# Optimization experiments

Measured on AMD Instinct MI355X. Metric: run time of the kernel, lower is better.

The kernel has to match this reference:

```python
import jax, jax.numpy as jnp
import numpy as np

HID = 32  # hidden channels (hard-coded in module)
K = 2     # kernel size


def conv1d(x, w, b, dilation=1):
    # x: [B, C_in, T], w: [C_out, C_in, K], b: [C_out]
    y = jax.lax.conv_general_dilated(
        x, w, window_strides=(1,), padding='VALID',
        rhs_dilation=(dilation,), dimension_numbers=('NCH', 'OIH', 'NCH'))
    return y + b[None, :, None]


def setup_inputs() -> dict:
    key = jax.random.key(0)
    ks = jax.random.split(key, 24)
    B, T, C_IN, C_OUT = 32, 4096, 64, 448
    s = 0.05
    inp = {
        'x': jax.random.normal(ks[0], (B, T, C_IN), dtype=jnp.float32),
        'w_causal': jax.random.normal(ks[1], (HID, C_IN, K), dtype=jnp.float32) * s,
        'b_causal': jax.random.normal(ks[2], (HID,), dtype=jnp.float32) * s,
        'wd0': jax.random.normal(ks[3], (HID, HID, K), dtype=jnp.float32) * s,
        'bd0': jax.random.normal(ks[4], (HID,), dtype=jnp.float32) * s,
        'ws0': jax.random.normal(ks[5], (HID, HID, 1), dtype=jnp.float32) * s,
        'bs0': jax.random.normal(ks[6], (HID,), dtype=jnp.float32) * s,
        'wo0': jax.random.normal(ks[7], (HID, HID, 1), dtype=jnp.float32) * s,
        'bo0': jax.random.normal(ks[8], (HID,), dtype=jnp.float32) * s,
        'wd1': jax.random.normal(ks[9], (HID, HID, K), dtype=jnp.float32) * s,
        'bd1': jax.random.normal(ks[10], (HID,), dtype=jnp.float32) * s,
        'ws1': jax.random.normal(ks[11], (HID, HID, 1), dtype=jnp.float32) * s,
        'bs1': jax.random.normal(ks[12], (HID,), dtype=jnp.float32) * s,
        'wo1': jax.random.normal(ks[13], (HID, HID, 1), dtype=jnp.float32) * s,
        'bo1': jax.random.normal(ks[14], (HID,), dtype=jnp.float32) * s,
        'w_sk1': jax.random.normal(ks[15], (HID, HID, 1), dtype=jnp.float32) * s,
        'b_sk1': jax.random.normal(ks[16], (HID,), dtype=jnp.float32) * s,
        'w_sk2': jax.random.normal(ks[17], (C_OUT, HID, 1), dtype=jnp.float32) * s,
        'b_sk2': jax.random.normal(ks[18], (C_OUT,), dtype=jnp.float32) * s,
    }
    return inp


def reference(x, w_causal, b_causal,
              wd0, bd0, ws0, bs0, wo0, bo0,
              wd1, bd1, ws1, bs1, wo1, bo1,
              w_sk1, b_sk1, w_sk2, b_sk2):
    # x: [B, T, C_in] -> [B, C_in, T]
    xt = jnp.transpose(x, (0, 2, 1))
    # T (=4096) >= rf_size (=4) so the top-level rf padding branch is a no-op.
    xt = jnp.pad(xt, ((0, 0), (0, 0), (1, 0)))  # causal left-pad of 1
    z = conv1d(xt, w_causal, b_causal)          # [B, HID, T]

    skip = jnp.zeros_like(z)
    blocks = [(wd0, bd0, ws0, bs0, wo0, bo0, 1),
              (wd1, bd1, ws1, bs1, wo1, bo1, 2)]
    for wd, bd, ws, bs, wo, bo, dil in blocks:
        zp = jnp.pad(z, ((0, 0), (0, 0), (dil, 0)))  # causal pad of `dilation`
        g = conv1d(zp, wd, bd, dilation=dil)          # length preserved: T
        g = jnp.tanh(g) * jax.nn.sigmoid(g)           # gated activation
        skip = skip + conv1d(g, ws, bs)               # skip accumulation
        z = conv1d(g, wo, bo) + z                     # residual (x[...,-T:] == z)

    out = jax.nn.relu(skip)
    out = jax.nn.relu(conv1d(out, w_sk1, b_sk1))
    out = conv1d(out, w_sk2, b_sk2)                   # [B, C_out, T]
    return jnp.transpose(out, (0, 2, 1))              # [B, T, C_out]
```

## Files before the change

kernel.cpp:

```cpp
#include <hip/hip_runtime.h>

#define T_LEN 4096
#define NB    32
#define CIN   64
#define CH    32
#define COUT  448
#define COLS  64
#define HALO  3
#define OUTC  (COLS - HALO)
#define BLK_A 256
#define TR_B  16

#define H_ELEMS  (NB * T_LEN * CH)
#define WT_C   0
#define WT_D0  4096
#define WT_D1  6144
#define WT_S0  8192
#define WT_O0  9216
#define WT_S1  10240
#define WT_K1  11264
#define WT_N   12288

__device__ __forceinline__ float gated(float d) {
  float dc = fminf(fmaxf(d, -30.0f), 30.0f);
  float e2 = __expf(-2.0f * dc);
  float th = (1.0f - e2) / (1.0f + e2);
  float sg = 1.0f / (1.0f + __expf(-dc));
  return th * sg;
}

__global__ void dicnn_prep(const float* __restrict__ wc,
    const float* __restrict__ wd0, const float* __restrict__ wd1,
    const float* __restrict__ ws0, const float* __restrict__ wo0,
    const float* __restrict__ ws1, const float* __restrict__ wk1,
    float* __restrict__ wt)
{
  int i = blockIdx.x * 256 + threadIdx.x;
  if (i >= WT_N) return;
  float v;
  if (i < WT_D0) {
    int c = i & 31, k = (i >> 5) & 1, ci = i >> 6;
    v = wc[c * 128 + ci * 2 + k];
  } else if (i < WT_D1) {
    int j = i - WT_D0; int c = j & 31, k = (j >> 5) & 1, ci = j >> 6;
    v = wd0[c * 64 + ci * 2 + k];
  } else if (i < WT_S0) {
    int j = i - WT_D1; int c = j & 31, k = (j >> 5) & 1, ci = j >> 6;
    v = wd1[c * 64 + ci * 2 + k];
  } else if (i < WT_O0) {
    int j = i - WT_S0; int c = j & 31, ci = j >> 5;
    v = ws0[c * 32 + ci];
  } else if (i < WT_S1) {
    int j = i - WT_O0; int c = j & 31, ci = j >> 5;
    v = wo0[c * 32 + ci];
  } else if (i < WT_K1) {
    int j = i - WT_S1; int c = j & 31, ci = j >> 5;
    v = ws1[c * 32 + ci];
  } else {
    int j = i - WT_K1; int c = j & 31, ci = j >> 5;
    v = wk1[c * 32 + ci];
  }
  wt[i] = v;
}

__global__ __launch_bounds__(BLK_A, 4) void dicnn_front(
    const float* __restrict__ x, const float* __restrict__ wt,
    const float* __restrict__ b_causal,
    const float* __restrict__ bd0, const float* __restrict__ bs0,
    const float* __restrict__ bo0, const float* __restrict__ bd1,
    const float* __restrict__ bs1, const float* __restrict__ b_sk1,
    float* __restrict__ h_out)
{
  __shared__ float zbuf[CH][COLS];
  __shared__ float gbuf[CH][COLS];

  const int tid = threadIdx.x;
  const int col = tid & 63;
  const int c0  = __builtin_amdgcn_readfirstlane((tid >> 6) << 3);
  const int b   = blockIdx.y;
  const int t   = blockIdx.x * OUTC - HALO + col;

  const float* wt_c  = wt + WT_C;
  const float* wt_d0 = wt + WT_D0;
  const float* wt_d1 = wt + WT_D1;
  const float* wt_s0 = wt + WT_S0;
  const float* wt_o0 = wt + WT_O0;
  const float* wt_s1 = wt + WT_S1;
  const float* wt_k1 = wt + WT_K1;

  float z0[8];
  #pragma unroll
  for (int c = 0; c < 8; ++c) z0[c] = 0.f;
  if (t >= 0 && t < T_LEN) {
    #pragma unroll
    for (int c = 0; c < 8; ++c) z0[c] = b_causal[c0 + c];
    const float* xr = x + ((size_t)b * T_LEN + t) * CIN;
    for (int ci = 0; ci < CIN; ci += 4) {
      float4 xc = *(const float4*)(xr + ci);
      float4 xp = make_float4(0.f, 0.f, 0.f, 0.f);
      if (t > 0) xp = *(const float4*)(xr - CIN + ci);
      #pragma unroll
      for (int j = 0; j < 4; ++j) {
        const float* wp = wt_c + (ci + j) * 64 + c0;
        const float xpv = (&xp.x)[j];
        const float xcv = (&xc.x)[j];
        #pragma unroll
        for (int c = 0; c < 8; ++c)
          z0[c] += wp[c] * xpv + wp[32 + c] * xcv;
      }
    }
  }
  #pragma unroll
  for (int c = 0; c < 8; ++c) zbuf[c0 + c][col] = z0[c];
  __syncthreads();

  const int cp1 = (col >= 1) ? col - 1 : 0;
  float acc[8];
  #pragma unroll
  for (int c = 0; c < 8; ++c) acc[c] = bd0[c0 + c];
  for (int ci = 0; ci < CH; ++ci) {
    float zp = zbuf[ci][cp1];
    float zc = zbuf[ci][col];
    const float* wp = wt_d0 + ci * 64 + c0;
    #pragma unroll
    for (int c = 0; c < 8; ++c)
      acc[c] += wp[c] * zp + wp[32 + c] * zc;
  }
  #pragma unroll
  for (int c = 0; c < 8; ++c) gbuf[c0 + c][col] = gated(acc[c]);
  __syncthreads();

  float skip[8], z1[8];
  #pragma unroll
  for (int c = 0; c < 8; ++c) { skip[c] = bs0[c0 + c]; z1[c] = z0[c] + bo0[c0 + c]; }
  for (int ci = 0; ci < CH; ++ci) {
    float gv = gbuf[ci][col];
    const float* wsp = wt_s0 + ci * 32 + c0;
    const float* wop = wt_o0 + ci * 32 + c0;
    #pragma unroll
    for (int c = 0; c < 8; ++c) { skip[c] += wsp[c] * gv; z1[c] += wop[c] * gv; }
  }
  if (t < 0) {
    #pragma unroll
    for (int c = 0; c < 8; ++c) z1[c] = 0.f;
  }
  #pragma unroll
  for (int c = 0; c < 8; ++c) zbuf[c0 + c][col] = z1[c];
  __syncthreads();

  const int cp2 = (col >= 2) ? col - 2 : 0;
  #pragma unroll
  for (int c = 0; c < 8; ++c) acc[c] = bd1[c0 + c];
  for (int ci = 0; ci < CH; ++ci) {
    float zp = zbuf[ci][cp2];
    float zc = zbuf[ci][col];
    const float* wp = wt_d1 + ci * 64 + c0;
    #pragma unroll
    for (int c = 0; c < 8; ++c)
      acc[c] += wp[c] * zp + wp[32 + c] * zc;
  }
  #pragma unroll
  for (int c = 0; c < 8; ++c) gbuf[c0 + c][col] = gated(acc[c]);
  __syncthreads();

  #pragma unroll
  for (int c = 0; c < 8; ++c) skip[c] += bs1[c0 + c];
  for (int ci = 0; ci < CH; ++ci) {
    float gv = gbuf[ci][col];
    const float* wsp = wt_s1 + ci * 32 + c0;
    #pragma unroll
    for (int c = 0; c < 8; ++c) skip[c] += wsp[c] * gv;
  }
  #pragma unroll
  for (int c = 0; c < 8; ++c) zbuf[c0 + c][col] = fmaxf(skip[c], 0.f);
  __syncthreads();

  float h[8];
  #pragma unroll
  for (int c = 0; c < 8; ++c) h[c] = b_sk1[c0 + c];
  for (int ci = 0; ci < CH; ++ci) {
    float rv = zbuf[ci][col];
    const float* wkp = wt_k1 + ci * 32 + c0;
    #pragma unroll
    for (int c = 0; c < 8; ++c) h[c] += wkp[c] * rv;
  }
  if (col >= HALO && t < T_LEN) {
    float* hr = h_out + ((size_t)b * T_LEN + t) * CH + c0;
    float4 v0 = make_float4(fmaxf(h[0], 0.f), fmaxf(h[1], 0.f),
                            fmaxf(h[2], 0.f), fmaxf(h[3], 0.f));
    float4 v1 = make_float4(fmaxf(h[4], 0.f), fmaxf(h[5], 0.f),
                            fmaxf(h[6], 0.f), fmaxf(h[7], 0.f));
    *(float4*)(hr)     = v0;
    *(float4*)(hr + 4) = v1;
  }
}

__global__ __launch_bounds__(COUT) void dicnn_out(
    const float* __restrict__ h, const float* __restrict__ w_sk2,
    const float* __restrict__ b_sk2, float* __restrict__ out)
{
  const int co = threadIdx.x;
  const size_t r0 = (size_t)blockIdx.x * TR_B;
  float w[CH];
  #pragma unroll
  for (int i = 0; i < CH; i += 4) {
    float4 v = *(const float4*)(w_sk2 + (size_t)co * CH + i);
    w[i] = v.x; w[i+1] = v.y; w[i+2] = v.z; w[i+3] = v.w;
  }
  const float bias = b_sk2[co];
  #pragma unroll 2
  for (int r = 0; r < TR_B; ++r) {
    const float* hr = h + (r0 + r) * CH;
    float a0 = bias, a1 = 0.f, a2 = 0.f, a3 = 0.f;
    #pragma unroll
    for (int i = 0; i < CH; i += 4) {
      float4 hv = *(const float4*)(hr + i);
      a0 += w[i]   * hv.x;  a1 += w[i+1] * hv.y;
      a2 += w[i+2] * hv.z;  a3 += w[i+3] * hv.w;
    }
    out[(r0 + r) * COUT + co] = (a0 + a1) + (a2 + a3);
  }
}

extern "C" void kernel_launch(void* const* d_in, const int* in_sizes, int n_in,
                              void* d_out, int out_size, void* d_ws, size_t ws_size,
                              hipStream_t stream) {
  (void)in_sizes; (void)n_in; (void)out_size; (void)ws_size;
  const float* x        = (const float*)d_in[0];
  const float* w_causal = (const float*)d_in[1];
  const float* b_causal = (const float*)d_in[2];
  const float* wd0      = (const float*)d_in[3];
  const float* bd0      = (const float*)d_in[4];
  const float* ws0      = (const float*)d_in[5];
  const float* bs0      = (const float*)d_in[6];
  const float* wo0      = (const float*)d_in[7];
  const float* bo0      = (const float*)d_in[8];
  const float* wd1      = (const float*)d_in[9];
  const float* bd1      = (const float*)d_in[10];
  const float* ws1      = (const float*)d_in[11];
  const float* bs1      = (const float*)d_in[12];
  const float* w_sk1    = (const float*)d_in[15];
  const float* b_sk1    = (const float*)d_in[16];
  const float* w_sk2    = (const float*)d_in[17];
  const float* b_sk2    = (const float*)d_in[18];
  float* out = (float*)d_out;
  float* hws = (float*)d_ws;
  float* wt  = (float*)d_ws + H_ELEMS;

  dicnn_prep<<<(WT_N + 255) / 256, 256, 0, stream>>>(
      w_causal, wd0, wd1, ws0, wo0, ws1, w_sk1, wt);

  dim3 gA((T_LEN + OUTC - 1) / OUTC, NB);
  dicnn_front<<<gA, BLK_A, 0, stream>>>(x, wt, b_causal,
      bd0, bs0, bo0, bd1, bs1, b_sk1, hws);

  dim3 gB((NB * T_LEN) / TR_B);
  dicnn_out<<<gB, COUT, 0, stream>>>(hws, w_sk2, b_sk2, out);
}
```

Measured before the change: 439.8 us.

## Process two time columns per thread in front kernel and enlarge output row tiles

The front kernel now covers 128 time columns per block: each thread computes two columns, so every weight load is reused for two outputs and the 3-column halo recompute is spread over more useful columns. The occupancy hint on the front kernel is dropped to leave room for the doubled register arrays. The output kernel processes 64 rows per block with deeper unrolling, which cuts per-block weight loading and launch overhead. The costs are more registers, lower occupancy and fewer blocks in both kernels.

```diff
diff --git a/kernel.cpp b/kernel.cpp
--- a/kernel.cpp
+++ b/kernel.cpp
@@ -5,11 +5,11 @@
 #define CIN   64
 #define CH    32
 #define COUT  448
-#define COLS  64
+#define COLS  128
 #define HALO  3
 #define OUTC  (COLS - HALO)
 #define BLK_A 256
-#define TR_B  16
+#define TR_B  64
 
 #define H_ELEMS  (NB * T_LEN * CH)
 #define WT_C   0
@@ -63,7 +63,7 @@
   wt[i] = v;
 }
 
-__global__ __launch_bounds__(BLK_A, 4) void dicnn_front(
+__global__ __launch_bounds__(BLK_A) void dicnn_front(
     const float* __restrict__ x, const float* __restrict__ wt,
     const float* __restrict__ b_causal,
     const float* __restrict__ bd0, const float* __restrict__ bs0,
@@ -75,10 +75,10 @@
   __shared__ float gbuf[CH][COLS];
 
   const int tid = threadIdx.x;
-  const int col = tid & 63;
+  const int cp  = tid & 63;
   const int c0  = __builtin_amdgcn_readfirstlane((tid >> 6) << 3);
   const int b   = blockIdx.y;
-  const int t   = blockIdx.x * OUTC - HALO + col;
+  const int tA  = blockIdx.x * OUTC - HALO + cp;
 
   const float* wt_c  = wt + WT_C;
   const float* wt_d0 = wt + WT_D0;
@@ -88,110 +88,152 @@
   const float* wt_s1 = wt + WT_S1;
   const float* wt_k1 = wt + WT_K1;
 
-  float z0[8];
-  #pragma unroll
-  for (int c = 0; c < 8; ++c) z0[c] = 0.f;
-  if (t >= 0 && t < T_LEN) {
-    #pragma unroll
-    for (int c = 0; c < 8; ++c) z0[c] = b_causal[c0 + c];
-    const float* xr = x + ((size_t)b * T_LEN + t) * CIN;
-    for (int ci = 0; ci < CIN; ci += 4) {
-      float4 xc = *(const float4*)(xr + ci);
-      float4 xp = make_float4(0.f, 0.f, 0.f, 0.f);
-      if (t > 0) xp = *(const float4*)(xr - CIN + ci);
+  float z0[2][8];
+  #pragma unroll
+  for (int u = 0; u < 2; ++u) {
+    const int t = tA + u * 64;
+    #pragma unroll
+    for (int c = 0; c < 8; ++c) z0[u][c] = 0.f;
+    if (t >= 0 && t < T_LEN) {
       #pragma unroll
-      for (int j = 0; j < 4; ++j) {
-        const float* wp = wt_c + (ci + j) * 64 + c0;
-        const float xpv = (&xp.x)[j];
-        const float xcv = (&xc.x)[j];
+      for (int c = 0; c < 8; ++c) z0[u][c] = b_causal[c0 + c];
+      const float* xr = x + ((size_t)b * T_LEN + t) * CIN;
+      for (int ci = 0; ci < CIN; ci += 4) {
+        float4 xc = *(const float4*)(xr + ci);
+        float4 xp = make_float4(0.f, 0.f, 0.f, 0.f);
+        if (t > 0) xp = *(const float4*)(xr - CIN + ci);
         #pragma unroll
-        for (int c = 0; c < 8; ++c)
-          z0[c] += wp[c] * xpv + wp[32 + c] * xcv;
+        for (int j = 0; j < 4; ++j) {
+          const float* wp = wt_c + (ci + j) * 64 + c0;
+          const float xpv = (&xp.x)[j];
+          const float xcv = (&xc.x)[j];
+          #pragma unroll
+          for (int c = 0; c < 8; ++c)
+            z0[u][c] += wp[c] * xpv + wp[32 + c] * xcv;
+        }
       }
     }
-  }
-  #pragma unroll
-  for (int c = 0; c < 8; ++c) zbuf[c0 + c][col] = z0[c];
-  __syncthreads();
-
-  const int cp1 = (col >= 1) ? col - 1 : 0;
-  float acc[8];
-  #pragma unroll
-  for (int c = 0; c < 8; ++c) acc[c] = bd0[c0 + c];
-  for (int ci = 0; ci < CH; ++ci) {
-    float zp = zbuf[ci][cp1];
-    float zc = zbuf[ci][col];
+    #pragma unroll
+    for (int c = 0; c < 8; ++c) zbuf[c0 + c][cp + u * 64] = z0[u][c];
+  }
+  __syncthreads();
+
+  const int cA1 = (cp >= 1) ? cp - 1 : 0;
+  const int cB1 = cp + 63;
+  float acc[2][8];
+  #pragma unroll
+  for (int c = 0; c < 8; ++c) { acc[0][c] = bd0[c0 + c]; acc[1][c] = acc[0][c]; }
+  for (int ci = 0; ci < CH; ++ci) {
+    float zpA = zbuf[ci][cA1], zcA = zbuf[ci][cp];
+    float zpB = zbuf[ci][cB1], zcB = zbuf[ci][cp + 64];
     const float* wp = wt_d0 + ci * 64 + c0;
     #pragma unroll
-    for (int c = 0; c < 8; ++c)
-      acc[c] += wp[c] * zp + wp[32 + c] * zc;
-  }
-  #pragma unroll
-  for (int c = 0; c < 8; ++c) gbuf[c0 + c][col] = gated(acc[c]);
-  __syncthreads();
-
-  float skip[8], z1[8];
-  #pragma unroll
-  for (int c = 0; c < 8; ++c) { skip[c] = bs0[c0 + c]; z1[c] = z0[c] + bo0[c0 + c]; }
-  for (int ci = 0; ci < CH; ++ci) {
-    float gv = gbuf[ci][col];
+    for (int c = 0; c < 8; ++c) {
+      const float w0 = wp[c], w1 = wp[32 + c];
+      acc[0][c] += w0 * zpA + w1 * zcA;
+      acc[1][c] += w0 * zpB + w1 * zcB;
+    }
+  }
+  #pragma unroll
+  for (int u = 0; u < 2; ++u)
+    #pragma unroll
+    for (int c = 0; c < 8; ++c) gbuf[c0 + c][cp + u * 64] = gated(acc[u][c]);
+  __syncthreads();
+
+  float skip[2][8], z1[2][8];
+  #pragma unroll
+  for (int c = 0; c < 8; ++c) {
+    const float bs = bs0[c0 + c], bo = bo0[c0 + c];
+    skip[0][c] = bs;              skip[1][c] = bs;
+    z1[0][c] = z0[0][c] + bo;     z1[1][c] = z0[1][c] + bo;
+  }
+  for (int ci = 0; ci < CH; ++ci) {
+    float gA = gbuf[ci][cp], gB = gbuf[ci][cp + 64];
     const float* wsp = wt_s0 + ci * 32 + c0;
     const float* wop = wt_o0 + ci * 32 + c0;
     #pragma unroll
-    for (int c = 0; c < 8; ++c) { skip[c] += wsp[c] * gv; z1[c] += wop[c] * gv; }
-  }
-  if (t < 0) {
-    #pragma unroll
-    for (int c = 0; c < 8; ++c) z1[c] = 0.f;
-  }
-  #pragma unroll
-  for (int c = 0; c < 8; ++c) zbuf[c0 + c][col] = z1[c];
-  __syncthreads();
-
-  const int cp2 = (col >= 2) ? col - 2 : 0;
-  #pragma unroll
-  for (int c = 0; c < 8; ++c) acc[c] = bd1[c0 + c];
-  for (int ci = 0; ci < CH; ++ci) {
-    float zp = zbuf[ci][cp2];
-    float zc = zbuf[ci][col];
+    for (int c = 0; c < 8; ++c) {
+      const float ws = wsp[c], wo = wop[c];
+      skip[0][c] += ws * gA;  z1[0][c] += wo * gA;
+      skip[1][c] += ws * gB;  z1[1][c] += wo * gB;
+    }
+  }
+  if (tA < 0) {
+    #pragma unroll
+    for (int c = 0; c < 8; ++c) z1[0][c] = 0.f;
+  }
+  #pragma unroll
+  for (int u = 0; u < 2; ++u)
+    #pragma unroll
+    for (int c = 0; c < 8; ++c) zbuf[c0 + c][cp + u * 64] = z1[u][c];
+  __syncthreads();
+
+  const int cA2 = (cp >= 2) ? cp - 2 : 0;
+  const int cB2 = cp + 62;
+  #pragma unroll
+  for (int c = 0; c < 8; ++c) { acc[0][c] = bd1[c0 + c]; acc[1][c] = acc[0][c]; }
+  for (int ci = 0; ci < CH; ++ci) {
+    float zpA = zbuf[ci][cA2], zcA = zbuf[ci][cp];
+    float zpB = zbuf[ci][cB2], zcB = zbuf[ci][cp + 64];
     const float* wp = wt_d1 + ci * 64 + c0;
     #pragma unroll
-    for (int c = 0; c < 8; ++c)
-      acc[c] += wp[c] * zp + wp[32 + c] * zc;
-  }
-  #pragma unroll
-  for (int c = 0; c < 8; ++c) gbuf[c0 + c][col] = gated(acc[c]);
-  __syncthreads();
-
-  #pragma unroll
-  for (int c = 0; c < 8; ++c) skip[c] += bs1[c0 + c];
-  for (int ci = 0; ci < CH; ++ci) {
-    float gv = gbuf[ci][col];
+    for (int c = 0; c < 8; ++c) {
+      const float w0 = wp[c], w1 = wp[32 + c];
+      acc[0][c] += w0 * zpA + w1 * zcA;
+      acc[1][c] += w0 * zpB + w1 * zcB;
+    }
+  }
+  #pragma unroll
+  for (int u = 0; u < 2; ++u)
+    #pragma unroll
+    for (int c = 0; c < 8; ++c) gbuf[c0 + c][cp + u * 64] = gated(acc[u][c]);
+  __syncthreads();
+
+  #pragma unroll
+  for (int c = 0; c < 8; ++c) {
+    const float bs = bs1[c0 + c];
+    skip[0][c] += bs; skip[1][c] += bs;
+  }
+  for (int ci = 0; ci < CH; ++ci) {
+    float gA = gbuf[ci][cp], gB = gbuf[ci][cp + 64];
     const float* wsp = wt_s1 + ci * 32 + c0;
     #pragma unroll
-    for (int c = 0; c < 8; ++c) skip[c] += wsp[c] * gv;
-  }
-  #pragma unroll
-  for (int c = 0; c < 8; ++c) zbuf[c0 + c][col] = fmaxf(skip[c], 0.f);
-  __syncthreads();
-
-  float h[8];
-  #pragma unroll
-  for (int c = 0; c < 8; ++c) h[c] = b_sk1[c0 + c];
-  for (int ci = 0; ci < CH; ++ci) {
-    float rv = zbuf[ci][col];
+    for (int c = 0; c < 8; ++c) {
+      const float ws = wsp[c];
+      skip[0][c] += ws * gA;  skip[1][c] += ws * gB;
+    }
+  }
+  #pragma unroll
+  for (int u = 0; u < 2; ++u)
+    #pragma unroll
+    for (int c = 0; c < 8; ++c) zbuf[c0 + c][cp + u * 64] = fmaxf(skip[u][c], 0.f);
+  __syncthreads();
+
+  float h[2][8];
+  #pragma unroll
+  for (int c = 0; c < 8; ++c) { h[0][c] = b_sk1[c0 + c]; h[1][c] = h[0][c]; }
+  for (int ci = 0; ci < CH; ++ci) {
+    float rA = zbuf[ci][cp], rB = zbuf[ci][cp + 64];
     const float* wkp = wt_k1 + ci * 32 + c0;
     #pragma unroll
-    for (int c = 0; c < 8; ++c) h[c] += wkp[c] * rv;
-  }
-  if (col >= HALO && t < T_LEN) {
-    float* hr = h_out + ((size_t)b * T_LEN + t) * CH + c0;
-    float4 v0 = make_float4(fmaxf(h[0], 0.f), fmaxf(h[1], 0.f),
-                            fmaxf(h[2], 0.f), fmaxf(h[3], 0.f));
-    float4 v1 = make_float4(fmaxf(h[4], 0.f), fmaxf(h[5], 0.f),
-                            fmaxf(h[6], 0.f), fmaxf(h[7], 0.f));
-    *(float4*)(hr)     = v0;
-    *(float4*)(hr + 4) = v1;
+    for (int c = 0; c < 8; ++c) {
+      const float wk = wkp[c];
+      h[0][c] += wk * rA;  h[1][c] += wk * rB;
+    }
+  }
+  #pragma unroll
+  for (int u = 0; u < 2; ++u) {
+    const int col = cp + u * 64;
+    const int t   = tA + u * 64;
+    if (col >= HALO && t < T_LEN) {
+      float* hr = h_out + ((size_t)b * T_LEN + t) * CH + c0;
+      float4 v0 = make_float4(fmaxf(h[u][0], 0.f), fmaxf(h[u][1], 0.f),
+                              fmaxf(h[u][2], 0.f), fmaxf(h[u][3], 0.f));
+      float4 v1 = make_float4(fmaxf(h[u][4], 0.f), fmaxf(h[u][5], 0.f),
+                              fmaxf(h[u][6], 0.f), fmaxf(h[u][7], 0.f));
+      *(float4*)(hr)     = v0;
+      *(float4*)(hr + 4) = v1;
+    }
   }
 }
 
@@ -208,7 +250,7 @@
     w[i] = v.x; w[i+1] = v.y; w[i+2] = v.z; w[i+3] = v.w;
   }
   const float bias = b_sk2[co];
-  #pragma unroll 2
+  #pragma unroll 8
   for (int r = 0; r < TR_B; ++r) {
     const float* hr = h + (r0 + r) * CH;
     float a0 = bias, a1 = 0.f, a2 = 0.f, a3 = 0.f;
```

New measurement: 462.5 us. 5.1% more time.
